# Kernel optimization log

Measured on AMD Instinct MI355X. Metric: run time of the kernel, lower is better.

The kernel has to match this reference:

```python
import jax, jax.numpy as jnp
import numpy as np

NUM_CAMS = 1
NUM_HEADS = 1
NUM_LEVELS = 1
NUM_POINTS = 4
NUM_DEPTH = 128
EMBED = 128  # must equal NUM_DEPTH (output_proj is applied to the depth axis)


def setup_inputs() -> dict:
    key0 = jax.random.key(0)
    ks = jax.random.split(key0, 12)
    bsv, nq, nv = 1, 1024, 1024  # nq == nv == H*W (32*32)
    off_dim = NUM_CAMS * NUM_HEADS * NUM_LEVELS * NUM_DEPTH * NUM_POINTS * 2  # 1024
    aw_dim = NUM_CAMS * NUM_HEADS * NUM_LEVELS * NUM_DEPTH * NUM_POINTS       # 512
    return {
        "query": jax.random.normal(ks[0], (bsv, nq, EMBED), jnp.float32),
        "key": jax.random.normal(ks[1], (NUM_CAMS, nv, bsv, EMBED), jnp.float32),
        "value": jax.random.normal(ks[2], (NUM_CAMS, nv, bsv, EMBED), jnp.float32),
        "ref_3d": jax.random.uniform(ks[3], (bsv * NUM_CAMS, nq * NUM_DEPTH, 2), jnp.float32),
        "spatial_shapes": jnp.array([[32, 32]], dtype=jnp.int32),
        "W_off": jax.random.normal(ks[4], (EMBED, off_dim), jnp.float32) * 0.02,
        "b_off": jax.random.normal(ks[5], (off_dim,), jnp.float32) * 0.02,
        "W_attn": jax.random.normal(ks[6], (EMBED, aw_dim), jnp.float32) * 0.02,
        "b_attn": jax.random.normal(ks[7], (aw_dim,), jnp.float32) * 0.02,
        "W_v": jax.random.normal(ks[8], (EMBED, EMBED), jnp.float32) / np.sqrt(EMBED),
        "b_v": jnp.zeros((EMBED,), jnp.float32),
        "W_o": jax.random.normal(ks[9], (EMBED, EMBED), jnp.float32) / np.sqrt(EMBED),
        "b_o": jnp.zeros((EMBED,), jnp.float32),
    }


def _bilinear_sample(val, H, W, x, y):
    """grid_sample(align_corners=False, padding=zeros) equivalent.
    val: [B, H*W, D]; x, y: [B, Q, P] in pixel coords. Returns [B, Q, P, D]."""
    B, Q, P = x.shape
    D = val.shape[-1]
    x0f = jnp.floor(x); y0f = jnp.floor(y)
    ix0 = x0f.astype(jnp.int32); iy0 = y0f.astype(jnp.int32)
    wx1 = x - x0f; wy1 = y - y0f
    wx0 = 1.0 - wx1; wy0 = 1.0 - wy1

    def corner(ix, iy, w):
        valid = (ix >= 0) & (ix < W) & (iy >= 0) & (iy < H)
        idx = jnp.clip(iy, 0, H - 1) * W + jnp.clip(ix, 0, W - 1)  # [B,Q,P]
        g = jnp.take_along_axis(val, idx.reshape(B, Q * P)[:, :, None], axis=1)
        g = g.reshape(B, Q, P, D)
        return g * (w * valid.astype(val.dtype))[..., None]

    return (corner(ix0, iy0, wx0 * wy0)
            + corner(ix0 + 1, iy0, wx1 * wy0)
            + corner(ix0, iy0 + 1, wx0 * wy1)
            + corner(ix0 + 1, iy0 + 1, wx1 * wy1))


def reference(query, key, value, ref_3d, spatial_shapes,
              W_off, b_off, W_attn, b_attn, W_v, b_v, W_o, b_o):
    bsv, nq, E = query.shape
    cams, nv, bs, _ = key.shape
    identity = query

    # key/value: [cams, nv, bs, E] -> [bsv, nv, E]
    key2 = jnp.transpose(key, (2, 0, 1, 3)).reshape(bsv, nv, E)
    val = jnp.flip(value, axis=0)
    val = jnp.transpose(val, (2, 0, 1, 3)).reshape(bsv, nv, E)
    val = val @ W_v + b_v
    val = val.reshape(bsv * cams, nv, E)  # num_heads=1 -> head_dim=E

    # offsets / attention weights (heads=levels=1 axes squeezed)
    off = (query @ W_off + b_off).reshape(bsv, nq, cams, NUM_DEPTH, NUM_POINTS, 2)
    aw = (query @ W_attn + b_attn).reshape(bsv, nq, cams, NUM_DEPTH, NUM_LEVELS * NUM_POINTS)
    aw = jax.nn.softmax(aw, axis=-1).reshape(bsv, nq, cams, NUM_DEPTH, NUM_POINTS)
    off = jnp.transpose(off, (0, 2, 1, 3, 4, 5)).reshape(bsv * cams, nq * NUM_DEPTH, NUM_POINTS, 2)
    aw = jnp.transpose(aw, (0, 2, 1, 3, 4)).reshape(bsv * cams, nq * NUM_DEPTH, NUM_POINTS)

    H = spatial_shapes[0, 0]
    W = spatial_shapes[0, 1]
    norm = jnp.stack([W, H]).astype(off.dtype)  # [W, H]
    loc = ref_3d[:, :, None, :] + off / norm    # [B, Qe, P, 2] in [0,1]
    x = loc[..., 0] * W.astype(loc.dtype) - 0.5
    y = loc[..., 1] * H.astype(loc.dtype) - 0.5

    sampled = _bilinear_sample(val, H, W, x, y)          # [B, Qe, P, E]
    out = jnp.einsum('bqpe,bqp->bqe', sampled, aw)       # weighted sum over points

    out = out.reshape(bsv, cams, nq, NUM_DEPTH, E).mean(axis=1)  # [bsv, nq, depth, E]
    out = (out * key2[:, :, None, :]).mean(axis=-1)              # [bsv, nq, depth]
    out = out @ W_o + b_o                                        # depth == EMBED
    return out + identity  # dropout = identity in eval
```

## Files before the change

kernel.cpp:

```cpp
#include <hip/hip_runtime.h>
#include <hip/hip_bf16.h>


#define NQ   1024
#define NV   1024
#define E    128
#define ND   128
#define NP   4
#define IMG_W 32
#define IMG_H 32

__global__ __launch_bounds__(256) void gemm_nn_k128(
    const float* __restrict__ A, const float* __restrict__ B,
    const float* __restrict__ bias, const float* __restrict__ add,
    float* __restrict__ C, int M, int N) {
  __shared__ float As[64][129];
  __shared__ float Bs[128][64];

  const int tid = threadIdx.x;
  const int tx = tid & 15, ty = tid >> 4;
  const int n0 = blockIdx.x * 64, m0 = blockIdx.y * 64;

  for (int k = 0; k < 8; ++k) {
    int c = tid + k * 256;
    int r = c >> 5;
    int e4 = c & 31;
    const float4 v = *(const float4*)(A + (size_t)(m0 + r) * 128 + e4 * 4);
    As[r][e4 * 4 + 0] = v.x; As[r][e4 * 4 + 1] = v.y;
    As[r][e4 * 4 + 2] = v.z; As[r][e4 * 4 + 3] = v.w;
  }
  for (int k = 0; k < 8; ++k) {
    int c = tid + k * 256;
    int e = c >> 4;
    int n4 = c & 15;
    *(float4*)(&Bs[e][n4 * 4]) = *(const float4*)(B + (size_t)e * N + n0 + n4 * 4);
  }
  __syncthreads();

  float acc[4][4] = {};
#pragma unroll 8
  for (int e = 0; e < 128; ++e) {
    const float a0 = As[ty * 4 + 0][e];
    const float a1 = As[ty * 4 + 1][e];
    const float a2 = As[ty * 4 + 2][e];
    const float a3 = As[ty * 4 + 3][e];
    const float4 b = *(const float4*)(&Bs[e][tx * 4]);
    acc[0][0] += a0 * b.x; acc[0][1] += a0 * b.y; acc[0][2] += a0 * b.z; acc[0][3] += a0 * b.w;
    acc[1][0] += a1 * b.x; acc[1][1] += a1 * b.y; acc[1][2] += a1 * b.z; acc[1][3] += a1 * b.w;
    acc[2][0] += a2 * b.x; acc[2][1] += a2 * b.y; acc[2][2] += a2 * b.z; acc[2][3] += a2 * b.w;
    acc[3][0] += a3 * b.x; acc[3][1] += a3 * b.y; acc[3][2] += a3 * b.z; acc[3][3] += a3 * b.w;
  }

#pragma unroll
  for (int i = 0; i < 4; ++i) {
    const int m = m0 + ty * 4 + i;
    const int n = n0 + tx * 4;
    float4 r;
    r.x = acc[i][0]; r.y = acc[i][1]; r.z = acc[i][2]; r.w = acc[i][3];
    if (bias) {
      r.x += bias[n + 0]; r.y += bias[n + 1]; r.z += bias[n + 2]; r.w += bias[n + 3];
    }
    if (add) {
      const float4 ad = *(const float4*)(add + (size_t)m * N + n);
      r.x += ad.x; r.y += ad.y; r.z += ad.z; r.w += ad.w;
    }
    *(float4*)(C + (size_t)m * N + n) = r;
  }
}

__global__ __launch_bounds__(256) void gemm_nt_k128(
    const float* __restrict__ A, const float* __restrict__ Bt,
    float* __restrict__ C, int M, int N) {
  __shared__ float As[64][129];
  __shared__ float Bs[64][129];

  const int tid = threadIdx.x;
  const int tx = tid & 15, ty = tid >> 4;
  const int n0 = blockIdx.x * 64, m0 = blockIdx.y * 64;

  for (int k = 0; k < 8; ++k) {
    int c = tid + k * 256;
    int r = c >> 5;
    int e4 = c & 31;
    const float4 va = *(const float4*)(A + (size_t)(m0 + r) * 128 + e4 * 4);
    As[r][e4 * 4 + 0] = va.x; As[r][e4 * 4 + 1] = va.y;
    As[r][e4 * 4 + 2] = va.z; As[r][e4 * 4 + 3] = va.w;
    const float4 vb = *(const float4*)(Bt + (size_t)(n0 + r) * 128 + e4 * 4);
    Bs[r][e4 * 4 + 0] = vb.x; Bs[r][e4 * 4 + 1] = vb.y;
    Bs[r][e4 * 4 + 2] = vb.z; Bs[r][e4 * 4 + 3] = vb.w;
  }
  __syncthreads();

  float acc[4][4] = {};
#pragma unroll 8
  for (int e = 0; e < 128; ++e) {
    const float a0 = As[ty * 4 + 0][e];
    const float a1 = As[ty * 4 + 1][e];
    const float a2 = As[ty * 4 + 2][e];
    const float a3 = As[ty * 4 + 3][e];
    const float b0 = Bs[tx * 4 + 0][e];
    const float b1 = Bs[tx * 4 + 1][e];
    const float b2 = Bs[tx * 4 + 2][e];
    const float b3 = Bs[tx * 4 + 3][e];
    acc[0][0] += a0 * b0; acc[0][1] += a0 * b1; acc[0][2] += a0 * b2; acc[0][3] += a0 * b3;
    acc[1][0] += a1 * b0; acc[1][1] += a1 * b1; acc[1][2] += a1 * b2; acc[1][3] += a1 * b3;
    acc[2][0] += a2 * b0; acc[2][1] += a2 * b1; acc[2][2] += a2 * b2; acc[2][3] += a2 * b3;
    acc[3][0] += a3 * b0; acc[3][1] += a3 * b1; acc[3][2] += a3 * b2; acc[3][3] += a3 * b3;
  }

#pragma unroll
  for (int i = 0; i < 4; ++i) {
    const int m = m0 + ty * 4 + i;
    const int n = n0 + tx * 4;
    float4 r;
    r.x = acc[i][0]; r.y = acc[i][1]; r.z = acc[i][2]; r.w = acc[i][3];
    *(float4*)(C + (size_t)m * N + n) = r;
  }
}

__global__ __launch_bounds__(256) void sample_kernel(
    const float* __restrict__ dotv,
    const float* __restrict__ off,
    const float* __restrict__ awr,
    const float* __restrict__ ref3d,
    float* __restrict__ out1) {
  __shared__ float img[2][NV];

  const int tid = threadIdx.x;
  const int q0 = blockIdx.x * 2;

  for (int k = 0; k < 2; ++k) {
    int c = tid + k * 256;
    int qq = c >> 8;
    int v4 = c & 255;
    *(float4*)(&img[qq][v4 * 4]) =
        *(const float4*)(dotv + (size_t)(q0 + qq) * NV + v4 * 4);
  }
  __syncthreads();

  const int qq = tid >> 7;
  const int q = q0 + qq;
  const int d = tid & 127;
  const float* im = img[qq];
  const size_t qe = (size_t)q * ND + d;

  const float rx = ref3d[qe * 2 + 0];
  const float ry = ref3d[qe * 2 + 1];

  const float* awp = awr + (size_t)q * (ND * NP) + d * NP;
  const float a0 = awp[0], a1 = awp[1], a2 = awp[2], a3 = awp[3];
  const float mx = fmaxf(fmaxf(a0, a1), fmaxf(a2, a3));
  const float e0 = __expf(a0 - mx), e1 = __expf(a1 - mx),
              e2 = __expf(a2 - mx), e3 = __expf(a3 - mx);
  const float inv = 1.0f / (e0 + e1 + e2 + e3);
  float w[4] = {e0 * inv, e1 * inv, e2 * inv, e3 * inv};

  const float* op = off + (size_t)q * (ND * NP * 2) + d * (NP * 2);

  float acc = 0.0f;
#pragma unroll
  for (int p = 0; p < NP; ++p) {
    const float x = rx * (float)IMG_W + op[p * 2 + 0] - 0.5f;
    const float y = ry * (float)IMG_H + op[p * 2 + 1] - 0.5f;
    const float xf = floorf(x), yf = floorf(y);
    const int ix0 = (int)xf, iy0 = (int)yf;
    const float wx1 = x - xf, wy1 = y - yf;
    const float wx0 = 1.0f - wx1, wy0 = 1.0f - wy1;

    float s = 0.0f;
#pragma unroll
    for (int cy = 0; cy < 2; ++cy) {
#pragma unroll
      for (int cx = 0; cx < 2; ++cx) {
        const int ix = ix0 + cx, iy = iy0 + cy;
        const bool valid = (ix >= 0) & (ix < IMG_W) & (iy >= 0) & (iy < IMG_H);
        const int cix = min(max(ix, 0), IMG_W - 1);
        const int ciy = min(max(iy, 0), IMG_H - 1);
        const float wgt = (cx ? wx1 : wx0) * (cy ? wy1 : wy0);
        s += valid ? im[ciy * IMG_W + cix] * wgt : 0.0f;
      }
    }
    acc += w[p] * s;
  }
  out1[qe] = acc * (1.0f / (float)E);
}

extern "C" void kernel_launch(void* const* d_in, const int* in_sizes, int n_in,
                              void* d_out, int out_size, void* d_ws, size_t ws_size,
                              hipStream_t stream) {
  const float* query  = (const float*)d_in[0];
  const float* key    = (const float*)d_in[1];
  const float* value  = (const float*)d_in[2];
  const float* ref3d  = (const float*)d_in[3];
  const float* W_off  = (const float*)d_in[5];
  const float* b_off  = (const float*)d_in[6];
  const float* W_attn = (const float*)d_in[7];
  const float* b_attn = (const float*)d_in[8];
  const float* W_v    = (const float*)d_in[9];
  const float* b_v    = (const float*)d_in[10];
  const float* W_o    = (const float*)d_in[11];
  const float* b_o    = (const float*)d_in[12];
  float* out = (float*)d_out;

  float* ws = (float*)d_ws;
  float* off_out = ws;
  float* aw_out  = off_out + (size_t)NQ * 1024;
  float* val2    = aw_out + (size_t)NQ * 512;
  float* dotv    = val2 + (size_t)NV * E;
  float* out1    = dotv + (size_t)NQ * NV;

  gemm_nn_k128<<<dim3(1024 / 64, NQ / 64), 256, 0, stream>>>(
      query, W_off, b_off, nullptr, off_out, NQ, 1024);
  gemm_nn_k128<<<dim3(512 / 64, NQ / 64), 256, 0, stream>>>(
      query, W_attn, b_attn, nullptr, aw_out, NQ, 512);
  gemm_nn_k128<<<dim3(128 / 64, NV / 64), 256, 0, stream>>>(
      value, W_v, b_v, nullptr, val2, NV, 128);
  gemm_nt_k128<<<dim3(NV / 64, NQ / 64), 256, 0, stream>>>(
      key, val2, dotv, NQ, NV);
  sample_kernel<<<NQ / 2, 256, 0, stream>>>(dotv, off_out, aw_out, ref3d, out1);
  gemm_nn_k128<<<dim3(128 / 64, NQ / 64), 256, 0, stream>>>(
      out1, W_o, b_o, query, out, NQ, 128);
}
```

Before: 122.4 us.

## Merge projection GEMMs into one launch, reassociate key-value product, fuse output proj

The three independent projection GEMMs (offsets, attention weights, and a key·W_v^T projection) plus a key·b_v bias vector now run as one grouped launch. The key-value dot product is reassociated as (key·W_v^T)·value^T plus a per-row bias term, so the value projection no longer needs its own stage. The output projection and residual add are folded into the sampling kernel, and the shared-memory tiles are stored transposed so the inner loop reads float4 vectors. This removes three launches and the out1 round trip through memory, at the cost of a serial per-thread bias-dot block and an uncoalesced W_o read inside the sampler.

```diff
diff --git a/kernel.cpp b/kernel.cpp
--- a/kernel.cpp
+++ b/kernel.cpp
@@ -4,185 +4,204 @@
 
 #define NQ   1024
 #define NV   1024
-#define E    128
 #define ND   128
 #define NP   4
 #define IMG_W 32
 #define IMG_H 32
 
-__global__ __launch_bounds__(256) void gemm_nn_k128(
-    const float* __restrict__ A, const float* __restrict__ B,
-    const float* __restrict__ bias, const float* __restrict__ add,
-    float* __restrict__ C, int M, int N) {
-  __shared__ float As[64][129];
-  __shared__ float Bs[128][64];
-
+__device__ __forceinline__ void gemm_tile64(
+    const float* __restrict__ A,
+    const float* __restrict__ B,
+    int N, bool nt,
+    const float* __restrict__ bias,
+    const float* __restrict__ cvec,
+    float* __restrict__ C,
+    int m0, int n0, float* sA, float* sB) {
   const int tid = threadIdx.x;
-  const int tx = tid & 15, ty = tid >> 4;
-  const int n0 = blockIdx.x * 64, m0 = blockIdx.y * 64;
-
+
+#pragma unroll
   for (int k = 0; k < 8; ++k) {
     int c = tid + k * 256;
-    int r = c >> 5;
-    int e4 = c & 31;
-    const float4 v = *(const float4*)(A + (size_t)(m0 + r) * 128 + e4 * 4);
-    As[r][e4 * 4 + 0] = v.x; As[r][e4 * 4 + 1] = v.y;
-    As[r][e4 * 4 + 2] = v.z; As[r][e4 * 4 + 3] = v.w;
-  }
-  for (int k = 0; k < 8; ++k) {
-    int c = tid + k * 256;
-    int e = c >> 4;
-    int n4 = c & 15;
-    *(float4*)(&Bs[e][n4 * 4]) = *(const float4*)(B + (size_t)e * N + n0 + n4 * 4);
+    int m = c & 63, e4 = c >> 6;
+    const float4 v = *(const float4*)(A + (size_t)(m0 + m) * 128 + e4 * 4);
+    sA[(e4 * 4 + 0) * 64 + m] = v.x;
+    sA[(e4 * 4 + 1) * 64 + m] = v.y;
+    sA[(e4 * 4 + 2) * 64 + m] = v.z;
+    sA[(e4 * 4 + 3) * 64 + m] = v.w;
+  }
+  if (nt) {
+#pragma unroll
+    for (int k = 0; k < 8; ++k) {
+      int c = tid + k * 256;
+      int n = c & 63, e4 = c >> 6;
+      const float4 v = *(const float4*)(B + (size_t)(n0 + n) * 128 + e4 * 4);
+      sB[(e4 * 4 + 0) * 64 + n] = v.x;
+      sB[(e4 * 4 + 1) * 64 + n] = v.y;
+      sB[(e4 * 4 + 2) * 64 + n] = v.z;
+      sB[(e4 * 4 + 3) * 64 + n] = v.w;
+    }
+  } else {
+#pragma unroll
+    for (int k = 0; k < 8; ++k) {
+      int c = tid + k * 256;
+      int n4 = c & 15, e = c >> 4;
+      *(float4*)(sB + e * 64 + n4 * 4) =
+          *(const float4*)(B + (size_t)e * N + n0 + n4 * 4);
+    }
   }
   __syncthreads();
 
+  const int tx = tid & 15, ty = tid >> 4;
   float acc[4][4] = {};
 #pragma unroll 8
   for (int e = 0; e < 128; ++e) {
-    const float a0 = As[ty * 4 + 0][e];
-    const float a1 = As[ty * 4 + 1][e];
-    const float a2 = As[ty * 4 + 2][e];
-    const float a3 = As[ty * 4 + 3][e];
-    const float4 b = *(const float4*)(&Bs[e][tx * 4]);
-    acc[0][0] += a0 * b.x; acc[0][1] += a0 * b.y; acc[0][2] += a0 * b.z; acc[0][3] += a0 * b.w;
-    acc[1][0] += a1 * b.x; acc[1][1] += a1 * b.y; acc[1][2] += a1 * b.z; acc[1][3] += a1 * b.w;
-    acc[2][0] += a2 * b.x; acc[2][1] += a2 * b.y; acc[2][2] += a2 * b.z; acc[2][3] += a2 * b.w;
-    acc[3][0] += a3 * b.x; acc[3][1] += a3 * b.y; acc[3][2] += a3 * b.z; acc[3][3] += a3 * b.w;
-  }
-
+    const float4 a = *(const float4*)(sA + e * 64 + ty * 4);
+    const float4 b = *(const float4*)(sB + e * 64 + tx * 4);
+    acc[0][0] += a.x * b.x; acc[0][1] += a.x * b.y; acc[0][2] += a.x * b.z; acc[0][3] += a.x * b.w;
+    acc[1][0] += a.y * b.x; acc[1][1] += a.y * b.y; acc[1][2] += a.y * b.z; acc[1][3] += a.y * b.w;
+    acc[2][0] += a.z * b.x; acc[2][1] += a.z * b.y; acc[2][2] += a.z * b.z; acc[2][3] += a.z * b.w;
+    acc[3][0] += a.w * b.x; acc[3][1] += a.w * b.y; acc[3][2] += a.w * b.z; acc[3][3] += a.w * b.w;
+  }
+
+  float4 bv = make_float4(0.f, 0.f, 0.f, 0.f);
+  if (bias) bv = *(const float4*)(bias + n0 + tx * 4);
 #pragma unroll
   for (int i = 0; i < 4; ++i) {
     const int m = m0 + ty * 4 + i;
-    const int n = n0 + tx * 4;
+    float cv = cvec ? cvec[m] : 0.f;
     float4 r;
-    r.x = acc[i][0]; r.y = acc[i][1]; r.z = acc[i][2]; r.w = acc[i][3];
-    if (bias) {
-      r.x += bias[n + 0]; r.y += bias[n + 1]; r.z += bias[n + 2]; r.w += bias[n + 3];
-    }
-    if (add) {
-      const float4 ad = *(const float4*)(add + (size_t)m * N + n);
-      r.x += ad.x; r.y += ad.y; r.z += ad.z; r.w += ad.w;
-    }
-    *(float4*)(C + (size_t)m * N + n) = r;
-  }
-}
-
-__global__ __launch_bounds__(256) void gemm_nt_k128(
-    const float* __restrict__ A, const float* __restrict__ Bt,
-    float* __restrict__ C, int M, int N) {
-  __shared__ float As[64][129];
-  __shared__ float Bs[64][129];
-
-  const int tid = threadIdx.x;
-  const int tx = tid & 15, ty = tid >> 4;
-  const int n0 = blockIdx.x * 64, m0 = blockIdx.y * 64;
-
-  for (int k = 0; k < 8; ++k) {
-    int c = tid + k * 256;
-    int r = c >> 5;
-    int e4 = c & 31;
-    const float4 va = *(const float4*)(A + (size_t)(m0 + r) * 128 + e4 * 4);
-    As[r][e4 * 4 + 0] = va.x; As[r][e4 * 4 + 1] = va.y;
-    As[r][e4 * 4 + 2] = va.z; As[r][e4 * 4 + 3] = va.w;
-    const float4 vb = *(const float4*)(Bt + (size_t)(n0 + r) * 128 + e4 * 4);
-    Bs[r][e4 * 4 + 0] = vb.x; Bs[r][e4 * 4 + 1] = vb.y;
-    Bs[r][e4 * 4 + 2] = vb.z; Bs[r][e4 * 4 + 3] = vb.w;
-  }
-  __syncthreads();
-
-  float acc[4][4] = {};
-#pragma unroll 8
-  for (int e = 0; e < 128; ++e) {
-    const float a0 = As[ty * 4 + 0][e];
-    const float a1 = As[ty * 4 + 1][e];
-    const float a2 = As[ty * 4 + 2][e];
-    const float a3 = As[ty * 4 + 3][e];
-    const float b0 = Bs[tx * 4 + 0][e];
-    const float b1 = Bs[tx * 4 + 1][e];
-    const float b2 = Bs[tx * 4 + 2][e];
-    const float b3 = Bs[tx * 4 + 3][e];
-    acc[0][0] += a0 * b0; acc[0][1] += a0 * b1; acc[0][2] += a0 * b2; acc[0][3] += a0 * b3;
-    acc[1][0] += a1 * b0; acc[1][1] += a1 * b1; acc[1][2] += a1 * b2; acc[1][3] += a1 * b3;
-    acc[2][0] += a2 * b0; acc[2][1] += a2 * b1; acc[2][2] += a2 * b2; acc[2][3] += a2 * b3;
-    acc[3][0] += a3 * b0; acc[3][1] += a3 * b1; acc[3][2] += a3 * b2; acc[3][3] += a3 * b3;
-  }
-
-#pragma unroll
-  for (int i = 0; i < 4; ++i) {
-    const int m = m0 + ty * 4 + i;
-    const int n = n0 + tx * 4;
-    float4 r;
-    r.x = acc[i][0]; r.y = acc[i][1]; r.z = acc[i][2]; r.w = acc[i][3];
-    *(float4*)(C + (size_t)m * N + n) = r;
-  }
-}
-
-__global__ __launch_bounds__(256) void sample_kernel(
+    r.x = acc[i][0] + bv.x + cv;
+    r.y = acc[i][1] + bv.y + cv;
+    r.z = acc[i][2] + bv.z + cv;
+    r.w = acc[i][3] + bv.w + cv;
+    *(float4*)(C + (size_t)m * N + n0 + tx * 4) = r;
+  }
+}
+
+__global__ __launch_bounds__(256, 2) void p1_kernel(
+    const float* __restrict__ query, const float* __restrict__ key,
+    const float* __restrict__ W_off, const float* __restrict__ b_off,
+    const float* __restrict__ W_attn, const float* __restrict__ b_attn,
+    const float* __restrict__ W_v, const float* __restrict__ b_v,
+    float* __restrict__ off_ws, float* __restrict__ aw_ws,
+    float* __restrict__ keyp_ws, float* __restrict__ c_ws) {
+  __shared__ float sA[128 * 64];
+  __shared__ float sB[128 * 64];
+  const int t = blockIdx.x;
+  if (t < 256) {
+    gemm_tile64(query, W_off, 1024, false, b_off, nullptr, off_ws,
+                (t >> 4) * 64, (t & 15) * 64, sA, sB);
+  } else if (t < 384) {
+    const int u = t - 256;
+    gemm_tile64(query, W_attn, 512, false, b_attn, nullptr, aw_ws,
+                (u >> 3) * 64, (u & 7) * 64, sA, sB);
+  } else if (t < 416) {
+    const int u = t - 384;
+    gemm_tile64(key, W_v, 128, true, nullptr, nullptr, keyp_ws,
+                (u >> 1) * 64, (u & 1) * 64, sA, sB);
+  } else {
+    for (int i = 0; i < 4; ++i) {
+      const int q = threadIdx.x + i * 256;
+      float s = 0.f;
+      for (int e = 0; e < 128; ++e) s += key[(size_t)q * 128 + e] * b_v[e];
+      c_ws[q] = s;
+    }
+  }
+}
+
+__global__ __launch_bounds__(256, 2) void p2_kernel(
+    const float* __restrict__ keyp_ws, const float* __restrict__ value,
+    const float* __restrict__ c_ws, float* __restrict__ dotv_ws) {
+  __shared__ float sA[128 * 64];
+  __shared__ float sB[128 * 64];
+  const int t = blockIdx.x;
+  gemm_tile64(keyp_ws, value, 1024, true, nullptr, c_ws, dotv_ws,
+              (t >> 4) * 64, (t & 15) * 64, sA, sB);
+}
+
+__global__ __launch_bounds__(256) void p3_kernel(
     const float* __restrict__ dotv,
     const float* __restrict__ off,
     const float* __restrict__ awr,
     const float* __restrict__ ref3d,
-    float* __restrict__ out1) {
+    const float* __restrict__ query,
+    const float* __restrict__ W_o,
+    const float* __restrict__ b_o,
+    float* __restrict__ out) {
   __shared__ float img[2][NV];
+  __shared__ float o1s[2][ND];
 
   const int tid = threadIdx.x;
   const int q0 = blockIdx.x * 2;
 
+#pragma unroll
   for (int k = 0; k < 2; ++k) {
     int c = tid + k * 256;
-    int qq = c >> 8;
-    int v4 = c & 255;
+    int qq = c >> 8, v4 = c & 255;
     *(float4*)(&img[qq][v4 * 4]) =
         *(const float4*)(dotv + (size_t)(q0 + qq) * NV + v4 * 4);
   }
   __syncthreads();
 
-  const int qq = tid >> 7;
-  const int q = q0 + qq;
-  const int d = tid & 127;
-  const float* im = img[qq];
-  const size_t qe = (size_t)q * ND + d;
-
-  const float rx = ref3d[qe * 2 + 0];
-  const float ry = ref3d[qe * 2 + 1];
-
-  const float* awp = awr + (size_t)q * (ND * NP) + d * NP;
-  const float a0 = awp[0], a1 = awp[1], a2 = awp[2], a3 = awp[3];
-  const float mx = fmaxf(fmaxf(a0, a1), fmaxf(a2, a3));
-  const float e0 = __expf(a0 - mx), e1 = __expf(a1 - mx),
-              e2 = __expf(a2 - mx), e3 = __expf(a3 - mx);
-  const float inv = 1.0f / (e0 + e1 + e2 + e3);
-  float w[4] = {e0 * inv, e1 * inv, e2 * inv, e3 * inv};
-
-  const float* op = off + (size_t)q * (ND * NP * 2) + d * (NP * 2);
-
-  float acc = 0.0f;
-#pragma unroll
-  for (int p = 0; p < NP; ++p) {
-    const float x = rx * (float)IMG_W + op[p * 2 + 0] - 0.5f;
-    const float y = ry * (float)IMG_H + op[p * 2 + 1] - 0.5f;
-    const float xf = floorf(x), yf = floorf(y);
-    const int ix0 = (int)xf, iy0 = (int)yf;
-    const float wx1 = x - xf, wy1 = y - yf;
-    const float wx0 = 1.0f - wx1, wy0 = 1.0f - wy1;
-
-    float s = 0.0f;
-#pragma unroll
-    for (int cy = 0; cy < 2; ++cy) {
-#pragma unroll
-      for (int cx = 0; cx < 2; ++cx) {
-        const int ix = ix0 + cx, iy = iy0 + cy;
-        const bool valid = (ix >= 0) & (ix < IMG_W) & (iy >= 0) & (iy < IMG_H);
-        const int cix = min(max(ix, 0), IMG_W - 1);
-        const int ciy = min(max(iy, 0), IMG_H - 1);
-        const float wgt = (cx ? wx1 : wx0) * (cy ? wy1 : wy0);
-        s += valid ? im[ciy * IMG_W + cix] * wgt : 0.0f;
+  {
+    const int qq = tid >> 7;
+    const int q = q0 + qq;
+    const int d = tid & 127;
+    const float* im = img[qq];
+    const size_t qe = (size_t)q * ND + d;
+
+    const float rx = ref3d[qe * 2 + 0];
+    const float ry = ref3d[qe * 2 + 1];
+
+    const float* awp = awr + (size_t)q * (ND * NP) + d * NP;
+    const float a0 = awp[0], a1 = awp[1], a2 = awp[2], a3 = awp[3];
+    const float mx = fmaxf(fmaxf(a0, a1), fmaxf(a2, a3));
+    const float e0 = __expf(a0 - mx), e1 = __expf(a1 - mx),
+                e2 = __expf(a2 - mx), e3 = __expf(a3 - mx);
+    const float inv = 1.0f / (e0 + e1 + e2 + e3);
+    const float w[4] = {e0 * inv, e1 * inv, e2 * inv, e3 * inv};
+
+    const float* op = off + (size_t)q * (ND * NP * 2) + d * (NP * 2);
+
+    float acc = 0.0f;
+#pragma unroll
+    for (int p = 0; p < NP; ++p) {
+      const float x = rx * (float)IMG_W + op[p * 2 + 0] - 0.5f;
+      const float y = ry * (float)IMG_H + op[p * 2 + 1] - 0.5f;
+      const float xf = floorf(x), yf = floorf(y);
+      const int ix0 = (int)xf, iy0 = (int)yf;
+      const float wx1 = x - xf, wy1 = y - yf;
+      const float wx0 = 1.0f - wx1, wy0 = 1.0f - wy1;
+
+      float s = 0.0f;
+#pragma unroll
+      for (int cy = 0; cy < 2; ++cy) {
+#pragma unroll
+        for (int cx = 0; cx < 2; ++cx) {
+          const int ix = ix0 + cx, iy = iy0 + cy;
+          const bool valid = (ix >= 0) & (ix < IMG_W) & (iy >= 0) & (iy < IMG_H);
+          const int cix = min(max(ix, 0), IMG_W - 1);
+          const int ciy = min(max(iy, 0), IMG_H - 1);
+          const float wgt = (cx ? wx1 : wx0) * (cy ? wy1 : wy0);
+          s += valid ? im[ciy * IMG_W + cix] * wgt : 0.0f;
+        }
       }
-    }
-    acc += w[p] * s;
-  }
-  out1[qe] = acc * (1.0f / (float)E);
+      acc += w[p] * s;
+    }
+    o1s[qq][d] = acc * (1.0f / 128.0f);
+  }
+  __syncthreads();
+
+  {
+    const int qq = tid >> 7;
+    const int q = q0 + qq;
+    const int n = tid & 127;
+    float acc = b_o[n] + query[(size_t)q * 128 + n];
+#pragma unroll 8
+    for (int d = 0; d < 128; ++d)
+      acc += o1s[qq][d] * W_o[(size_t)d * 128 + n];
+    out[(size_t)q * 128 + n] = acc;
+  }
 }
 
 extern "C" void kernel_launch(void* const* d_in, const int* in_sizes, int n_in,
@@ -203,21 +222,15 @@
   float* out = (float*)d_out;
 
   float* ws = (float*)d_ws;
-  float* off_out = ws;
-  float* aw_out  = off_out + (size_t)NQ * 1024;
-  float* val2    = aw_out + (size_t)NQ * 512;
-  float* dotv    = val2 + (size_t)NV * E;
-  float* out1    = dotv + (size_t)NQ * NV;
-
-  gemm_nn_k128<<<dim3(1024 / 64, NQ / 64), 256, 0, stream>>>(
-      query, W_off, b_off, nullptr, off_out, NQ, 1024);
-  gemm_nn_k128<<<dim3(512 / 64, NQ / 64), 256, 0, stream>>>(
-      query, W_attn, b_attn, nullptr, aw_out, NQ, 512);
-  gemm_nn_k128<<<dim3(128 / 64, NV / 64), 256, 0, stream>>>(
-      value, W_v, b_v, nullptr, val2, NV, 128);
-  gemm_nt_k128<<<dim3(NV / 64, NQ / 64), 256, 0, stream>>>(
-      key, val2, dotv, NQ, NV);
-  sample_kernel<<<NQ / 2, 256, 0, stream>>>(dotv, off_out, aw_out, ref3d, out1);
-  gemm_nn_k128<<<dim3(128 / 64, NQ / 64), 256, 0, stream>>>(
-      out1, W_o, b_o, query, out, NQ, 128);
-}
+  float* off_ws  = ws;
+  float* aw_ws   = off_ws + (size_t)NQ * 1024;
+  float* keyp_ws = aw_ws + (size_t)NQ * 512;
+  float* c_ws    = keyp_ws + (size_t)NQ * 128;
+  float* dotv_ws = c_ws + 1024;
+
+  p1_kernel<<<417, 256, 0, stream>>>(query, key, W_off, b_off, W_attn, b_attn,
+                                     W_v, b_v, off_ws, aw_ws, keyp_ws, c_ws);
+  p2_kernel<<<256, 256, 0, stream>>>(keyp_ws, value, c_ws, dotv_ws);
+  p3_kernel<<<512, 256, 0, stream>>>(dotv_ws, off_ws, aw_ws, ref3d, query,
+                                     W_o, b_o, out);
+}
```

After: 114.1 us. -6.8%, faster.
